# Kernel tuning notes

Hardware: AMD Instinct MI355X
Metric: run time of the kernel (lower is better)

The kernel has to match this reference:

```python
import jax, jax.numpy as jnp
import numpy as np
import math

PATCH = 41
NUM_ANG = 8
NUM_SPATIAL = 4
BIN_KSIZE = 2 * int(PATCH / (NUM_SPATIAL + 1))   # 16
BIN_STRIDE = PATCH // NUM_SPATIAL                # 10
BIN_PAD = BIN_KSIZE // 4                         # 4
CLIPVAL = 0.2
EPS = 1e-10
N = 8192


def _sift_pooling_kernel(ksize: int) -> np.ndarray:
    k2 = float(ksize) / 2.0
    xc2 = k2 - np.abs(np.arange(ksize, dtype=np.float32) + 0.5 - k2)
    return (np.outer(xc2, xc2) / k2 ** 2).astype(np.float32)


def _sift_weighting_kernel(ksize: int) -> np.ndarray:
    # Gauss, vlfeat sigma: sigma_mul_2 = ksize**2
    k2 = float(ksize) / 2.0
    ys = np.arange(ksize, dtype=np.float32)[:, None]
    xs = np.arange(ksize, dtype=np.float32)[None, :]
    disq = (ys - k2 + 0.5) ** 2 + (xs - k2 + 0.5) ** 2
    return np.exp(-disq / float(ksize ** 2)).astype(np.float32)


def setup_inputs() -> dict:
    key = jax.random.key(0)
    x = jax.random.normal(key, (N, 1, PATCH, PATCH), dtype=jnp.float32)
    gk = jnp.asarray(_sift_weighting_kernel(PATCH))   # [41,41]
    pk = jnp.asarray(_sift_pooling_kernel(BIN_KSIZE))  # [16,16]
    return {"x": x, "gk": gk, "pk": pk}


def _l2_normalize(v):
    return v / jnp.maximum(jnp.linalg.norm(v, axis=1, keepdims=True), 1e-12)


def reference(x, gk, pk):
    # gradients via replicate-pad + central difference (matches [-1,0,1] convs)
    xp = jnp.pad(x, ((0, 0), (0, 0), (0, 0), (1, 1)), mode='edge')
    gx = xp[..., 2:] - xp[..., :-2]
    yp = jnp.pad(x, ((0, 0), (0, 0), (1, 1), (0, 0)), mode='edge')
    gy = yp[:, :, 2:, :] - yp[:, :, :-2, :]

    mag = jnp.sqrt(gx * gx + gy * gy + EPS) * gk  # gaussian-weighted magnitude
    ori = jnp.arctan2(gy, gx + EPS)

    # soft angular binning
    o_big = (ori + 2.0 * math.pi) / (2.0 * math.pi) * NUM_ANG
    bo0f = jnp.floor(o_big)
    wo1 = o_big - bo0f
    bo0 = bo0f.astype(jnp.int32) % NUM_ANG
    bo1 = (bo0 + 1) % NUM_ANG
    # [N,1,P,P,nb]
    contrib = (jax.nn.one_hot(bo0, NUM_ANG, dtype=mag.dtype) * ((1.0 - wo1) * mag)[..., None]
               + jax.nn.one_hot(bo1, NUM_ANG, dtype=mag.dtype) * (wo1 * mag)[..., None])
    contrib = jnp.transpose(contrib[:, 0], (0, 3, 1, 2))  # [N,nb,P,P]

    # depthwise weighted spatial pooling (same triangular kernel per angular bin)
    kern = jnp.broadcast_to(pk[None, None], (NUM_ANG, 1, BIN_KSIZE, BIN_KSIZE))
    pooled = jax.lax.conv_general_dilated(
        contrib, kern,
        window_strides=(BIN_STRIDE, BIN_STRIDE),
        padding=[(BIN_PAD, BIN_PAD), (BIN_PAD, BIN_PAD)],
        feature_group_count=NUM_ANG,
        dimension_numbers=('NCHW', 'OIHW', 'NCHW'))  # [N,nb,4,4]

    desc = pooled.reshape(pooled.shape[0], -1)  # [N,128]
    desc = _l2_normalize(desc)
    desc = jnp.clip(desc, 0.0, CLIPVAL)
    desc = _l2_normalize(desc)
    # rootsift: sqrt of L1-normalized descriptor
    desc = desc / jnp.maximum(jnp.sum(jnp.abs(desc), axis=1, keepdims=True), 1e-12)
    return jnp.sqrt(desc + 1e-10)
```

## Files before the change

kernel.cpp:

```cpp
#include <hip/hip_runtime.h>
#include <hip/hip_fp16.h>
#include <math.h>

#define PATCH 41
#define PP 1681
#define NB 8
#define STRIDE 10
#define PAD 4
#define NTH 192
#define XR 51
#define HR 5

__device__ __forceinline__ constexpr float tri16(int k) {
    float d = (float)k + 0.5f - 8.0f;
    float a = d < 0.0f ? -d : d;
    return (8.0f - a) * 0.125f;
}

__device__ __forceinline__ uint4 pixel_contrib(float gx, float gy, float w) {
    float X = gx + 1e-10f;
    float mag = __builtin_amdgcn_sqrtf(fmaf(gx, gx, fmaf(gy, gy, 1e-10f))) * w;

    float ax = fabsf(X), ay = fabsf(gy);
    float mx = fmaxf(ax, ay), mn = fminf(ax, ay);
    float r = mn * __builtin_amdgcn_rcpf(fmaxf(mx, 1e-30f));
    float r2 = r * r;
    float a4 = fmaf(r2, -0.0149238f, 0.0670406f);
    a4 = fmaf(r2, a4, -0.1482457f);
    a4 = fmaf(r2, a4, 0.2464287f);
    a4 = fmaf(r2, a4, -0.4235106f);
    a4 = fmaf(r2, a4, 1.2732106f);
    a4 *= r;

    bool sw = ay > ax;
    bool xn = X < 0.0f;
    bool yn = gy < 0.0f;
    int q = (xn ? 2 : 0) + ((sw != xn) ? 1 : 0);
    int b0 = yn ? 7 - q : q;
    bool f = (sw != xn) != yn;
    float ma = a4 * mag;
    float mb = mag - ma;
    float v0 = f ? ma : mb;
    float v1 = f ? mb : ma;

    unsigned combo = __builtin_bit_cast(unsigned, __builtin_amdgcn_cvt_pkrtz(v0, v1));
    int sh = (b0 & 3) << 4;
    unsigned long long A = (unsigned long long)combo << sh;
    unsigned long long B = ((b0 & 3) == 3) ? (unsigned long long)(combo >> 16) : 0ull;
    bool lohalf = b0 < 4;
    unsigned long long lo = lohalf ? A : B;
    unsigned long long hi = lohalf ? B : A;
    uint4 cw;
    cw.x = (unsigned)lo; cw.y = (unsigned)(lo >> 32);
    cw.z = (unsigned)hi; cw.w = (unsigned)(hi >> 32);
    return cw;
}

__device__ __forceinline__ __half2 u2h2(unsigned v) {
    return __builtin_bit_cast(__half2, v);
}

__device__ __forceinline__ unsigned dpp_prev(unsigned v) {
    return (unsigned)__builtin_amdgcn_update_dpp(0, (int)v, 0x111, 0xF, 0xF, true);
}
__device__ __forceinline__ unsigned dpp_next(unsigned v) {
    return (unsigned)__builtin_amdgcn_update_dpp(0, (int)v, 0x101, 0xF, 0xF, true);
}

__global__ __launch_bounds__(NTH, 6) void sift_desc_kernel(
        const float* __restrict__ x,
        const float* __restrict__ gk,
        const float* __restrict__ pk,
        float* __restrict__ out)
{
    const int patch = blockIdx.x;
    const int t = threadIdx.x;

    __shared__ __align__(16) float s_xp[PATCH * XR];
    __shared__ __align__(16) float s_gc[48];
    __shared__ __align__(16) __half s_H[49 * HR * NB];
    __shared__ float s_desc[128];

    const float* xp = x + (size_t)patch * PP;
    {
        int i = t / PATCH;
        int j = t - i * PATCH;
        for (int p = t; p < PP; p += NTH) {
            s_xp[i * XR + j + 6] = xp[p];
            j += 28; i += 4;
            if (j >= PATCH) { j -= PATCH; i += 1; }
        }
    }
    for (int q = t; q < 41 * 9; q += NTH) {
        int i = q / 9;
        int c = q - i * 9;
        int j = (c < 6) ? (c - 6) : (c + 35);
        int jc = min(max(j, 0), PATCH - 1);
        s_xp[i * XR + j + 6] = xp[i * PATCH + jc];
    }
    if (t < 48) {
        float d = (float)(t - 20);
        float g = __builtin_amdgcn_exp2f(d * d * -8.582362e-4f);
        s_gc[t] = (t < PATCH) ? g : 0.0f;
    }
    if (t < 160) {
        int dw = (t < 80) ? t : (820 + t);
        ((unsigned*)s_H)[dw] = 0u;
    }
    __syncthreads();

    if (t < PATCH * 4) {
        const int row = t >> 2;
        const int ox = t & 3;
        const int cb = ox * STRIDE;
        const int rowM = row * XR + cb + 6;
        const int rowU = (row > 0 ? row - 1 : 0) * XR + cb + 6;
        const int rowD = (row < PATCH - 1 ? row + 1 : PATCH - 1) * XR + cb + 6;

        float drow = (float)(row - 20);
        const float rf = __builtin_amdgcn_exp2f(drow * drow * -8.582362e-4f);

        float m[13], u[11], d[11], w[11];
        #pragma unroll
        for (int i = 0; i < 13; ++i) m[i] = s_xp[rowM - 1 + i];
        #pragma unroll
        for (int i = 0; i < 11; ++i) u[i] = s_xp[rowU + i];
        #pragma unroll
        for (int i = 0; i < 11; ++i) d[i] = s_xp[rowD + i];
        #pragma unroll
        for (int i = 0; i < 11; ++i) w[i] = s_gc[cb + i] * rf;

        const __half2 z2 = __float2half2_rn(0.0f);
        __half2 a0 = z2, a1 = z2, a2 = z2, a3 = z2;

        const bool ox0 = (ox == 0);
        const bool ox3 = (ox == 3);
        const __half2 wl[4] = {
            ox0 ? z2 : __float2half2_rn(tri16(0)),
            ox0 ? z2 : __float2half2_rn(tri16(1)),
            ox0 ? z2 : __float2half2_rn(tri16(2)),
            ox0 ? z2 : __float2half2_rn(tri16(3))
        };

        #pragma unroll
        for (int k = 0; k <= 10; ++k) {
            uint4 cw = pixel_contrib(m[k + 2] - m[k], d[k] - u[k], w[k]);

            const __half2 wo = __float2half2_rn(tri16(k + 4));
            a0 = __hfma2(u2h2(cw.x), wo, a0);
            a1 = __hfma2(u2h2(cw.y), wo, a1);
            a2 = __hfma2(u2h2(cw.z), wo, a2);
            a3 = __hfma2(u2h2(cw.w), wo, a3);

            if (k == 1) {
                unsigned rx = dpp_next(cw.x);
                unsigned ry = dpp_next(cw.y);
                unsigned rz = dpp_next(cw.z);
                unsigned rw = dpp_next(cw.w);
                rx = ox3 ? 0u : rx;  ry = ox3 ? 0u : ry;
                rz = ox3 ? 0u : rz;  rw = ox3 ? 0u : rw;
                const __half2 wr = __float2half2_rn(tri16(15));
                a0 = __hfma2(u2h2(rx), wr, a0);
                a1 = __hfma2(u2h2(ry), wr, a1);
                a2 = __hfma2(u2h2(rz), wr, a2);
                a3 = __hfma2(u2h2(rw), wr, a3);
            }
            if (k >= 6 && k < 10) {
                const __half2 wk = wl[k - 6];
                a0 = __hfma2(u2h2(dpp_prev(cw.x)), wk, a0);
                a1 = __hfma2(u2h2(dpp_prev(cw.y)), wk, a1);
                a2 = __hfma2(u2h2(dpp_prev(cw.z)), wk, a2);
                a3 = __hfma2(u2h2(dpp_prev(cw.w)), wk, a3);
            }
        }

        uint4 hv;
        hv.x = __builtin_bit_cast(unsigned, a0);
        hv.y = __builtin_bit_cast(unsigned, a1);
        hv.z = __builtin_bit_cast(unsigned, a2);
        hv.w = __builtin_bit_cast(unsigned, a3);
        *(uint4*)&s_H[((row + 4) * HR + ox) * NB] = hv;
    }
    __syncthreads();

    if (t < 128) {
        int b = t >> 4;
        int oy = (t >> 2) & 3;
        int ox = t & 3;
        const __half* hp = &s_H[(oy * STRIDE * HR + ox) * NB + b];
        float v = 0.0f;
        #pragma unroll
        for (int ky = 0; ky < 16; ++ky) {
            v = fmaf(tri16(ky), __half2float(hp[ky * HR * NB]), v);
        }
        s_desc[t] = v;
    }
    __syncthreads();

    if (t < 64) {
        float a = s_desc[t];
        float b = s_desc[t + 64];

        float ss = fmaf(a, a, b * b);
        #pragma unroll
        for (int o = 32; o > 0; o >>= 1) ss += __shfl_xor(ss, o);
        float inv = 1.0f / fmaxf(__builtin_amdgcn_sqrtf(ss), 1e-12f);
        a = fminf(fmaxf(a * inv, 0.0f), 0.2f);
        b = fminf(fmaxf(b * inv, 0.0f), 0.2f);

        float ss2 = fmaf(a, a, b * b);
        #pragma unroll
        for (int o = 32; o > 0; o >>= 1) ss2 += __shfl_xor(ss2, o);
        float inv2 = 1.0f / fmaxf(__builtin_amdgcn_sqrtf(ss2), 1e-12f);
        a *= inv2; b *= inv2;

        float l1 = a + b;
        #pragma unroll
        for (int o = 32; o > 0; o >>= 1) l1 += __shfl_xor(l1, o);
        float invl = 1.0f / fmaxf(l1, 1e-12f);

        float* op = out + (size_t)patch * 128;
        op[t]      = __builtin_amdgcn_sqrtf(fmaf(a, invl, 1e-10f));
        op[t + 64] = __builtin_amdgcn_sqrtf(fmaf(b, invl, 1e-10f));
    }
}

extern "C" void kernel_launch(void* const* d_in, const int* in_sizes, int n_in,
                              void* d_out, int out_size, void* d_ws, size_t ws_size,
                              hipStream_t stream) {
    const float* x  = (const float*)d_in[0];
    const float* gk = (const float*)d_in[1];
    const float* pk = (const float*)d_in[2];
    float* out = (float*)d_out;
    const int n = in_sizes[0] / PP;
    sift_desc_kernel<<<n, NTH, 0, stream>>>(x, gk, pk, out);
}
```

Measured before the change: 116.4 us.

## Process four patches per block with double-buffered register-staged prefetch

Each block now handles four consecutive patches and prefetches the next patch from global memory into registers while computing the current one, then writes it to an alternate shared buffer. The padded shared layout and separate edge-fill pass are dropped, and boundary columns are handled with clamped indices instead. This targets global load latency and per-block setup overhead, at the cost of fewer blocks (less parallelism across the GPU), extra registers for staging, and more shared memory per block.

```diff
diff --git a/kernel.cpp b/kernel.cpp
--- a/kernel.cpp
+++ b/kernel.cpp
@@ -6,10 +6,10 @@
 #define PP 1681
 #define NB 8
 #define STRIDE 10
-#define PAD 4
 #define NTH 192
-#define XR 51
 #define HR 5
+#define PPB 4
+#define TAIL (PP - 8 * NTH)
 
 __device__ __forceinline__ constexpr float tri16(int k) {
     float d = (float)k + 0.5f - 8.0f;
@@ -71,157 +71,176 @@
         const float* __restrict__ x,
         const float* __restrict__ gk,
         const float* __restrict__ pk,
-        float* __restrict__ out)
+        float* __restrict__ out,
+        int n)
 {
-    const int patch = blockIdx.x;
     const int t = threadIdx.x;
-
-    __shared__ __align__(16) float s_xp[PATCH * XR];
+    const int base = blockIdx.x * PPB;
+
+    __shared__ __align__(16) float sA[PP];
+    __shared__ __align__(16) float sB[PP];
     __shared__ __align__(16) float s_gc[48];
     __shared__ __align__(16) __half s_H[49 * HR * NB];
     __shared__ float s_desc[128];
 
-    const float* xp = x + (size_t)patch * PP;
-    {
-        int i = t / PATCH;
-        int j = t - i * PATCH;
-        for (int p = t; p < PP; p += NTH) {
-            s_xp[i * XR + j + 6] = xp[p];
-            j += 28; i += 4;
-            if (j >= PATCH) { j -= PATCH; i += 1; }
-        }
-    }
-    for (int q = t; q < 41 * 9; q += NTH) {
-        int i = q / 9;
-        int c = q - i * 9;
-        int j = (c < 6) ? (c - 6) : (c + 35);
-        int jc = min(max(j, 0), PATCH - 1);
-        s_xp[i * XR + j + 6] = xp[i * PATCH + jc];
-    }
     if (t < 48) {
-        float d = (float)(t - 20);
-        float g = __builtin_amdgcn_exp2f(d * d * -8.582362e-4f);
+        float dd = (float)(t - 20);
+        float g = __builtin_amdgcn_exp2f(dd * dd * -8.582362e-4f);
         s_gc[t] = (t < PATCH) ? g : 0.0f;
     }
     if (t < 160) {
         int dw = (t < 80) ? t : (820 + t);
         ((unsigned*)s_H)[dw] = 0u;
     }
+
+    const int row = t >> 2;
+    const int ox  = t & 3;
+    const int cb  = ox * STRIDE;
+    const bool ox0 = (ox == 0);
+    const bool ox3 = (ox == 3);
+    const float drow = (float)(row - 20);
+    const float rf = __builtin_amdgcn_exp2f(drow * drow * -8.582362e-4f);
+    const __half2 z2 = __float2half2_rn(0.0f);
+    const __half2 wl[4] = {
+        ox0 ? z2 : __float2half2_rn(tri16(0)),
+        ox0 ? z2 : __float2half2_rn(tri16(1)),
+        ox0 ? z2 : __float2half2_rn(tri16(2)),
+        ox0 ? z2 : __float2half2_rn(tri16(3))
+    };
+    const int rb = row * PATCH + cb;
+    const int ru = (row > 0 ? row - 1 : 0) * PATCH + cb;
+    const int rd = (row < PATCH - 1 ? row + 1 : PATCH - 1) * PATCH + cb;
+
+    {
+        const float* gp = x + (size_t)base * PP;
+        float stg[9];
+        #pragma unroll
+        for (int it = 0; it < 8; ++it) stg[it] = gp[it * NTH + t];
+        stg[8] = (t < TAIL) ? gp[8 * NTH + t] : 0.0f;
+        #pragma unroll
+        for (int it = 0; it < 8; ++it) sA[it * NTH + t] = stg[it];
+        if (t < TAIL) sA[8 * NTH + t] = stg[8];
+    }
     __syncthreads();
 
-    if (t < PATCH * 4) {
-        const int row = t >> 2;
-        const int ox = t & 3;
-        const int cb = ox * STRIDE;
-        const int rowM = row * XR + cb + 6;
-        const int rowU = (row > 0 ? row - 1 : 0) * XR + cb + 6;
-        const int rowD = (row < PATCH - 1 ? row + 1 : PATCH - 1) * XR + cb + 6;
-
-        float drow = (float)(row - 20);
-        const float rf = __builtin_amdgcn_exp2f(drow * drow * -8.582362e-4f);
-
-        float m[13], u[11], d[11], w[11];
-        #pragma unroll
-        for (int i = 0; i < 13; ++i) m[i] = s_xp[rowM - 1 + i];
-        #pragma unroll
-        for (int i = 0; i < 11; ++i) u[i] = s_xp[rowU + i];
-        #pragma unroll
-        for (int i = 0; i < 11; ++i) d[i] = s_xp[rowD + i];
-        #pragma unroll
-        for (int i = 0; i < 11; ++i) w[i] = s_gc[cb + i] * rf;
-
-        const __half2 z2 = __float2half2_rn(0.0f);
-        __half2 a0 = z2, a1 = z2, a2 = z2, a3 = z2;
-
-        const bool ox0 = (ox == 0);
-        const bool ox3 = (ox == 3);
-        const __half2 wl[4] = {
-            ox0 ? z2 : __float2half2_rn(tri16(0)),
-            ox0 ? z2 : __float2half2_rn(tri16(1)),
-            ox0 ? z2 : __float2half2_rn(tri16(2)),
-            ox0 ? z2 : __float2half2_rn(tri16(3))
-        };
-
-        #pragma unroll
-        for (int k = 0; k <= 10; ++k) {
-            uint4 cw = pixel_contrib(m[k + 2] - m[k], d[k] - u[k], w[k]);
-
-            const __half2 wo = __float2half2_rn(tri16(k + 4));
-            a0 = __hfma2(u2h2(cw.x), wo, a0);
-            a1 = __hfma2(u2h2(cw.y), wo, a1);
-            a2 = __hfma2(u2h2(cw.z), wo, a2);
-            a3 = __hfma2(u2h2(cw.w), wo, a3);
-
-            if (k == 1) {
-                unsigned rx = dpp_next(cw.x);
-                unsigned ry = dpp_next(cw.y);
-                unsigned rz = dpp_next(cw.z);
-                unsigned rw = dpp_next(cw.w);
-                rx = ox3 ? 0u : rx;  ry = ox3 ? 0u : ry;
-                rz = ox3 ? 0u : rz;  rw = ox3 ? 0u : rw;
-                const __half2 wr = __float2half2_rn(tri16(15));
-                a0 = __hfma2(u2h2(rx), wr, a0);
-                a1 = __hfma2(u2h2(ry), wr, a1);
-                a2 = __hfma2(u2h2(rz), wr, a2);
-                a3 = __hfma2(u2h2(rw), wr, a3);
+    #pragma unroll
+    for (int pi = 0; pi < PPB; ++pi) {
+        if (base + pi >= n) break;
+        const float* sC = (pi & 1) ? sB : sA;
+        float*       sN = (pi & 1) ? sA : sB;
+        const bool hn = (pi + 1 < PPB) && (base + pi + 1 < n);
+
+        float stg[9];
+        if (hn) {
+            const float* gp = x + (size_t)(base + pi + 1) * PP;
+            #pragma unroll
+            for (int it = 0; it < 8; ++it) stg[it] = gp[it * NTH + t];
+            stg[8] = (t < TAIL) ? gp[8 * NTH + t] : 0.0f;
+        }
+        __builtin_amdgcn_sched_barrier(0);
+
+        if (t < PATCH * 4) {
+            float m[13], u[11], d[11], w[11];
+            m[0]  = sC[rb + (ox0 ? 0 : -1)];
+            #pragma unroll
+            for (int i = 1; i < 12; ++i) m[i] = sC[rb + i - 1];
+            m[12] = sC[rb + (ox3 ? 10 : 11)];
+            #pragma unroll
+            for (int i = 0; i < 11; ++i) u[i] = sC[ru + i];
+            #pragma unroll
+            for (int i = 0; i < 11; ++i) d[i] = sC[rd + i];
+            #pragma unroll
+            for (int i = 0; i < 11; ++i) w[i] = s_gc[cb + i] * rf;
+
+            __half2 a0 = z2, a1 = z2, a2 = z2, a3 = z2;
+
+            #pragma unroll
+            for (int k = 0; k <= 10; ++k) {
+                uint4 cw = pixel_contrib(m[k + 2] - m[k], d[k] - u[k], w[k]);
+
+                const __half2 wo = __float2half2_rn(tri16(k + 4));
+                a0 = __hfma2(u2h2(cw.x), wo, a0);
+                a1 = __hfma2(u2h2(cw.y), wo, a1);
+                a2 = __hfma2(u2h2(cw.z), wo, a2);
+                a3 = __hfma2(u2h2(cw.w), wo, a3);
+
+                if (k == 1) {
+                    unsigned rx = dpp_next(cw.x);
+                    unsigned ry = dpp_next(cw.y);
+                    unsigned rz = dpp_next(cw.z);
+                    unsigned rw = dpp_next(cw.w);
+                    rx = ox3 ? 0u : rx;  ry = ox3 ? 0u : ry;
+                    rz = ox3 ? 0u : rz;  rw = ox3 ? 0u : rw;
+                    const __half2 wr = __float2half2_rn(tri16(15));
+                    a0 = __hfma2(u2h2(rx), wr, a0);
+                    a1 = __hfma2(u2h2(ry), wr, a1);
+                    a2 = __hfma2(u2h2(rz), wr, a2);
+                    a3 = __hfma2(u2h2(rw), wr, a3);
+                }
+                if (k >= 6 && k < 10) {
+                    const __half2 wk = wl[k - 6];
+                    a0 = __hfma2(u2h2(dpp_prev(cw.x)), wk, a0);
+                    a1 = __hfma2(u2h2(dpp_prev(cw.y)), wk, a1);
+                    a2 = __hfma2(u2h2(dpp_prev(cw.z)), wk, a2);
+                    a3 = __hfma2(u2h2(dpp_prev(cw.w)), wk, a3);
+                }
             }
-            if (k >= 6 && k < 10) {
-                const __half2 wk = wl[k - 6];
-                a0 = __hfma2(u2h2(dpp_prev(cw.x)), wk, a0);
-                a1 = __hfma2(u2h2(dpp_prev(cw.y)), wk, a1);
-                a2 = __hfma2(u2h2(dpp_prev(cw.z)), wk, a2);
-                a3 = __hfma2(u2h2(dpp_prev(cw.w)), wk, a3);
+
+            uint4 hv;
+            hv.x = __builtin_bit_cast(unsigned, a0);
+            hv.y = __builtin_bit_cast(unsigned, a1);
+            hv.z = __builtin_bit_cast(unsigned, a2);
+            hv.w = __builtin_bit_cast(unsigned, a3);
+            *(uint4*)&s_H[((row + 4) * HR + ox) * NB] = hv;
+        }
+
+        if (hn) {
+            #pragma unroll
+            for (int it = 0; it < 8; ++it) sN[it * NTH + t] = stg[it];
+            if (t < TAIL) sN[8 * NTH + t] = stg[8];
+        }
+        __syncthreads();
+
+        if (t < 128) {
+            int b  = t >> 4;
+            int oy = (t >> 2) & 3;
+            int oxx = t & 3;
+            const __half* hp = &s_H[(oy * STRIDE * HR + oxx) * NB + b];
+            float v = 0.0f;
+            #pragma unroll
+            for (int ky = 0; ky < 16; ++ky) {
+                v = fmaf(tri16(ky), __half2float(hp[ky * HR * NB]), v);
             }
-        }
-
-        uint4 hv;
-        hv.x = __builtin_bit_cast(unsigned, a0);
-        hv.y = __builtin_bit_cast(unsigned, a1);
-        hv.z = __builtin_bit_cast(unsigned, a2);
-        hv.w = __builtin_bit_cast(unsigned, a3);
-        *(uint4*)&s_H[((row + 4) * HR + ox) * NB] = hv;
-    }
-    __syncthreads();
-
-    if (t < 128) {
-        int b = t >> 4;
-        int oy = (t >> 2) & 3;
-        int ox = t & 3;
-        const __half* hp = &s_H[(oy * STRIDE * HR + ox) * NB + b];
-        float v = 0.0f;
-        #pragma unroll
-        for (int ky = 0; ky < 16; ++ky) {
-            v = fmaf(tri16(ky), __half2float(hp[ky * HR * NB]), v);
-        }
-        s_desc[t] = v;
-    }
-    __syncthreads();
-
-    if (t < 64) {
-        float a = s_desc[t];
-        float b = s_desc[t + 64];
-
-        float ss = fmaf(a, a, b * b);
-        #pragma unroll
-        for (int o = 32; o > 0; o >>= 1) ss += __shfl_xor(ss, o);
-        float inv = 1.0f / fmaxf(__builtin_amdgcn_sqrtf(ss), 1e-12f);
-        a = fminf(fmaxf(a * inv, 0.0f), 0.2f);
-        b = fminf(fmaxf(b * inv, 0.0f), 0.2f);
-
-        float ss2 = fmaf(a, a, b * b);
-        #pragma unroll
-        for (int o = 32; o > 0; o >>= 1) ss2 += __shfl_xor(ss2, o);
-        float inv2 = 1.0f / fmaxf(__builtin_amdgcn_sqrtf(ss2), 1e-12f);
-        a *= inv2; b *= inv2;
-
-        float l1 = a + b;
-        #pragma unroll
-        for (int o = 32; o > 0; o >>= 1) l1 += __shfl_xor(l1, o);
-        float invl = 1.0f / fmaxf(l1, 1e-12f);
-
-        float* op = out + (size_t)patch * 128;
-        op[t]      = __builtin_amdgcn_sqrtf(fmaf(a, invl, 1e-10f));
-        op[t + 64] = __builtin_amdgcn_sqrtf(fmaf(b, invl, 1e-10f));
+            s_desc[t] = v;
+        }
+        __syncthreads();
+
+        if (t < 64) {
+            float a = s_desc[t];
+            float b = s_desc[t + 64];
+
+            float ss = fmaf(a, a, b * b);
+            #pragma unroll
+            for (int o = 32; o > 0; o >>= 1) ss += __shfl_xor(ss, o);
+            float inv = 1.0f / fmaxf(__builtin_amdgcn_sqrtf(ss), 1e-12f);
+            a = fminf(fmaxf(a * inv, 0.0f), 0.2f);
+            b = fminf(fmaxf(b * inv, 0.0f), 0.2f);
+
+            float ss2 = fmaf(a, a, b * b);
+            #pragma unroll
+            for (int o = 32; o > 0; o >>= 1) ss2 += __shfl_xor(ss2, o);
+            float inv2 = 1.0f / fmaxf(__builtin_amdgcn_sqrtf(ss2), 1e-12f);
+            a *= inv2; b *= inv2;
+
+            float l1 = a + b;
+            #pragma unroll
+            for (int o = 32; o > 0; o >>= 1) l1 += __shfl_xor(l1, o);
+            float invl = 1.0f / fmaxf(l1, 1e-12f);
+
+            float* op = out + (size_t)(base + pi) * 128;
+            op[t]      = __builtin_amdgcn_sqrtf(fmaf(a, invl, 1e-10f));
+            op[t + 64] = __builtin_amdgcn_sqrtf(fmaf(b, invl, 1e-10f));
+        }
     }
 }
 
@@ -233,5 +252,6 @@
     const float* pk = (const float*)d_in[2];
     float* out = (float*)d_out;
     const int n = in_sizes[0] / PP;
-    sift_desc_kernel<<<n, NTH, 0, stream>>>(x, gk, pk, out);
-}
+    const int grid = (n + PPB - 1) / PPB;
+    sift_desc_kernel<<<grid, NTH, 0, stream>>>(x, gk, pk, out, n);
+}
```

Result: faster. 108.9 us (-6.4%).
